# Kernel tuning notes

Measured on AMD Instinct MI355X. Metric: run time of the kernel, lower is better.

## Reference

```python
import jax, jax.numpy as jnp
import numpy as np
from jax import lax


def _conv(x, w):
    # x: [B,H,W,C], w: [kh,kw,Cin,Cout], stride 1, 'same' padding
    return lax.conv_general_dilated(x, w, window_strides=(1, 1), padding='SAME',
                                    dimension_numbers=('NHWC', 'HWIO', 'NHWC'))


def setup_inputs() -> dict:
    key = jax.random.key(0)
    ks = jax.random.split(key, 4)
    B, T, H, W, Cin, F = 16, 5, 256, 256, 3, 8
    return {
        'input_tensor': jax.random.normal(ks[0], (B, T, H, W, Cin), jnp.float32),
        'kernel': jax.random.normal(ks[1], (3, 3, Cin, 4 * F), jnp.float32) * 0.1,
        'recurrent_kernel': jax.random.normal(ks[2], (3, 3, F, 4 * F), jnp.float32) * 0.1,
        'bias': jnp.zeros((4 * F,), jnp.float32),
        'gamma': jnp.ones((F,), jnp.float32),
        'beta': jnp.zeros((F,), jnp.float32),
        'moving_mean': jnp.zeros((F,), jnp.float32),
        'moving_var': jnp.ones((F,), jnp.float32),
        'dense_w': jax.random.normal(ks[3], (F, 2), jnp.float32) * 0.1,
        'dense_b': jnp.zeros((2,), jnp.float32),
    }


def reference(input_tensor, kernel, recurrent_kernel, bias, gamma, beta,
              moving_mean, moving_var, dense_w, dense_b):
    B, T, H, W, Cin = input_tensor.shape
    F = recurrent_kernel.shape[2]
    xs = jnp.moveaxis(input_tensor, 1, 0)  # [T,B,H,W,Cin] time-major for scan
    h0 = jnp.zeros((B, H, W, F), input_tensor.dtype)

    def step(carry, x_t):
        h, c = carry
        # fused 4-gate pre-activations, Keras gate order: i, f, c(g), o
        z = _conv(x_t, kernel) + _conv(h, recurrent_kernel) + bias
        i, f, g, o = jnp.split(z, 4, axis=-1)
        i = jax.nn.sigmoid(i)
        f = jax.nn.sigmoid(f)
        g = jnp.tanh(g)
        o = jax.nn.sigmoid(o)
        c = f * c + i * g
        h = o * jnp.tanh(c)
        return (h, c), None

    (h, _), _ = lax.scan(step, (h0, h0), xs)  # return_sequences=False -> last h

    # BatchNormalization (inference, Keras eps=1e-3)
    eps = 1e-3
    x = (h - moving_mean) * lax.rsqrt(moving_var + eps) * gamma + beta
    # LeakyReLU, Keras default alpha=0.3
    x = jnp.where(x >= 0, x, 0.3 * x)
    # Dense(2) over channel dim
    return jnp.einsum('bhwf,fk->bhwk', x, dense_w) + dense_b
```

## Files before the change

kernel.cpp:

```cpp
#include <hip/hip_runtime.h>


#define BB  16
#define TT  5
#define HH  256
#define WW  256
#define CIN 3
#define FF  8
#define GG  32

#define TW  32
#define THT 16
#define LW  34
#define LH  18
#define NG  8

#define LOG2E 1.44269504088896340736f

typedef _Float16 half8  __attribute__((ext_vector_type(8)));
typedef _Float16 half4  __attribute__((ext_vector_type(4)));
typedef _Float16 half2t __attribute__((ext_vector_type(2)));
typedef float    floatx4 __attribute__((ext_vector_type(4)));

__device__ __forceinline__ float frcp(float x) { return __builtin_amdgcn_rcpf(x); }
__device__ __forceinline__ float sig2(float z)  { return frcp(1.0f + __builtin_amdgcn_exp2f(z)); }
__device__ __forceinline__ float tanh2(float z) { return 1.0f - 2.0f * frcp(1.0f + __builtin_amdgcn_exp2f(z)); }

#define MFMA(A, B, C) __builtin_amdgcn_mfma_f32_16x16x32_f16((A), (B), (C), 0, 0, 0)

__global__ void build_frags(const float* __restrict__ wk,
                            const float* __restrict__ wr,
                            _Float16* __restrict__ blob) {
    const int lane = threadIdx.x & 63;
    const int quad = lane >> 4, nlo = lane & 15;
    for (int chunk = 0; chunk < 5; ++chunk) {
        for (int nh = 0; nh < 2; ++nh) {
            const int n = nh * 16 + nlo;
            const float scale = (n >= 16 && n < 24) ? (2.0f * LOG2E) : (-LOG2E);
            const int frag = chunk * 2 + nh;
            _Float16* dhi = blob + ((size_t)frag * 64 + lane) * 8;
            _Float16* dlo = (chunk >= 2)
                ? blob + ((size_t)(10 + (chunk - 2) * 2 + nh) * 64 + lane) * 8
                : nullptr;
            for (int j = 0; j < 8; ++j) {
                const int k = quad * 8 + j;
                float w = 0.0f;
                if (chunk == 0) {
                    int tap = k >> 2, ci = k & 3;
                    if (ci < 3) w = wk[(tap * 3 + ci) * GG + n];
                } else if (chunk == 1) {
                    if (quad == 0 && j < 3) w = wk[(8 * 3 + j) * GG + n];
                } else {
                    int c = chunk - 2;
                    int tap = c * 4 + quad, ci = j;
                    if (tap < 9) w = wr[(tap * FF + ci) * GG + n];
                }
                w *= scale;
                _Float16 wh = (_Float16)w;
                dhi[j] = wh;
                if (dlo) dlo[j] = (_Float16)(w - (float)wh);
            }
        }
    }
}

template <int MODE>
__global__ __launch_bounds__(256, 2) void lstm_step(
    const float* __restrict__ xg,
    int t,
    const _Float16* __restrict__ blob,
    const float* __restrict__ bias,
    const _Float16* __restrict__ hin,
    _Float16* __restrict__ hout,
    _Float16* __restrict__ cbuf,
    const float* __restrict__ gamma, const float* __restrict__ beta,
    const float* __restrict__ mean,  const float* __restrict__ var,
    const float* __restrict__ dw,    const float* __restrict__ db,
    float* __restrict__ out)
{
    __shared__ half8 hls[LH * LW];
    __shared__ half4 xls[LH * LW];

    const int tid  = threadIdx.x;
    const int bx = blockIdx.x, by = blockIdx.y, b = blockIdx.z;
    const int lane = tid & 63, wave = tid >> 6;
    const int quad = lane >> 4, nlo = lane & 15;
    const bool lo8 = (nlo < 8);
    const int fc = nlo & 7;

    const int gidbase = (((b * (int)gridDim.y + by) * (int)gridDim.x + bx) * 4 + wave) * NG;

    half2t cpre[NG];
    if (MODE != 0) {
#pragma unroll
        for (int g = 0; g < NG; ++g)
            cpre[g] = ((const half2t*)cbuf)[(size_t)(gidbase + g) * 64 + lane];
    }

    half8 bfh[10], bfl[6];
#pragma unroll
    for (int i = 0; i < 10; ++i)
        bfh[i] = *(const half8*)(blob + ((size_t)i * 64 + lane) * 8);
#pragma unroll
    for (int i = 0; i < 6; ++i)
        bfl[i] = *(const half8*)(blob + ((size_t)(10 + i) * 64 + lane) * 8);

    const float bv0 = bias[nlo] * (-LOG2E);
    const float bv1 = bias[16 + nlo] * (lo8 ? 2.0f * LOG2E : -LOG2E);

    for (int l = tid; l < LH * LW; l += 256) {
        int r = l / LW, c = l - r * LW;
        int gy = by * THT + r - 1, gx = bx * TW + c - 1;
        half4 vh = {(_Float16)0, (_Float16)0, (_Float16)0, (_Float16)0};
        if ((unsigned)gy < HH && (unsigned)gx < WW) {
            const float* p = xg + (((size_t)(b * TT + t) * HH + gy) * WW + gx) * CIN;
            vh.x = (_Float16)p[0]; vh.y = (_Float16)p[1]; vh.z = (_Float16)p[2];
        }
        xls[l] = vh;
    }
    if (MODE != 0) {
        for (int l = tid; l < LH * LW; l += 256) {
            int r = l / LW, c = l - r * LW;
            int gy = by * THT + r - 1, gx = bx * TW + c - 1;
            half8 v = {(_Float16)0, (_Float16)0, (_Float16)0, (_Float16)0,
                       (_Float16)0, (_Float16)0, (_Float16)0, (_Float16)0};
            if ((unsigned)gy < HH && (unsigned)gx < WW)
                v = *(const half8*)(hin + ((size_t)(b * HH + gy) * WW + gx) * FF);
            hls[l] = v;
        }
    }
    __syncthreads();

    float bn_s = 0.f, bn_b = 0.f, dw0 = 0.f, dw1 = 0.f, db0 = 0.f, db1 = 0.f;
    if (MODE == 2) {
        bn_s = gamma[fc] * rsqrtf(var[fc] + 1e-3f);
        bn_b = beta[fc] - mean[fc] * bn_s;
        dw0 = dw[fc * 2 + 0]; dw1 = dw[fc * 2 + 1];
        db0 = db[0]; db1 = db[1];
    }

#pragma unroll
    for (int g = 0; g < NG; ++g) {
        const int lr  = wave * 4 + (g >> 1);
        const int gx0 = (g & 1) * 16;
        const int lc  = gx0 + nlo;

        const int t0 = 2 * quad, t1 = t0 + 1;
        half4 p = xls[(lr + t0 / 3) * LW + lc + t0 % 3];
        half4 q = xls[(lr + t1 / 3) * LW + lc + t1 % 3];
        half4 s = xls[(lr + 2) * LW + lc + 2];
        half8 a_xA = (half8){p.x, p.y, p.z, p.w, q.x, q.y, q.z, q.w};
        half8 a_xB = (half8){s.x, s.y, s.z, s.w, s.x, s.y, s.z, s.w};

        floatx4 acc0 = {bv0, bv0, bv0, bv0};
        floatx4 acc1 = {bv1, bv1, bv1, bv1};
        acc0 = MFMA(a_xA, bfh[0], acc0);  acc1 = MFMA(a_xA, bfh[1], acc1);
        acc0 = MFMA(a_xB, bfh[2], acc0);  acc1 = MFMA(a_xB, bfh[3], acc1);
        if (MODE != 0) {
#pragma unroll
            for (int c = 0; c < 3; ++c) {
                int tap = c * 4 + quad;
                if (tap > 8) tap = 8;
                half8 ah = hls[(lr + tap / 3) * LW + lc + tap % 3];
                acc0 = MFMA(ah, bfh[4 + c * 2], acc0);
                acc1 = MFMA(ah, bfh[5 + c * 2], acc1);
                acc0 = MFMA(ah, bfl[c * 2 + 0], acc0);
                acc1 = MFMA(ah, bfl[c * 2 + 1], acc1);
            }
        }

        float s0 = lo8 ? acc0[2] : acc0[0]; float r0 = __shfl_xor(s0, 8, 64);
        float s1 = lo8 ? acc0[3] : acc0[1]; float r1 = __shfl_xor(s1, 8, 64);
        float s2 = lo8 ? acc1[2] : acc1[0]; float r2 = __shfl_xor(s2, 8, 64);
        float s3 = lo8 ? acc1[3] : acc1[1]; float r3 = __shfl_xor(s3, 8, 64);

        const float zi0 = lo8 ? acc0[0] : r0, zi1 = lo8 ? acc0[1] : r1;
        const float zf0 = lo8 ? r0 : acc0[2], zf1 = lo8 ? r1 : acc0[3];
        const float zg0 = lo8 ? acc1[0] : r2, zg1 = lo8 ? acc1[1] : r3;
        const float zo0 = lo8 ? r2 : acc1[2], zo1 = lo8 ? r3 : acc1[3];

        float c0 = 0.f, c1 = 0.f;
        if (MODE != 0) { c0 = (float)cpre[g].x; c1 = (float)cpre[g].y; }

        const float ii0 = sig2(zi0), ff0 = sig2(zf0), gg0 = tanh2(zg0), oo0 = sig2(zo0);
        const float cn0 = ff0 * c0 + ii0 * gg0;
        const float hn0 = oo0 * tanh2(cn0 * (2.0f * LOG2E));
        const float ii1 = sig2(zi1), ff1 = sig2(zf1), gg1 = tanh2(zg1), oo1 = sig2(zo1);
        const float cn1 = ff1 * c1 + ii1 * gg1;
        const float hn1 = oo1 * tanh2(cn1 * (2.0f * LOG2E));

        const int m0 = quad * 4 + (lo8 ? 0 : 2);
        const int gy = by * THT + lr;
        if (MODE != 2) {
            half2t cc; cc.x = (_Float16)cn0; cc.y = (_Float16)cn1;
            ((half2t*)cbuf)[(size_t)(gidbase + g) * 64 + lane] = cc;
            _Float16* hp = hout + ((size_t)(b * HH + gy) * WW + bx * TW + gx0 + m0) * FF + fc;
            hp[0]  = (_Float16)hn0;
            hp[FF] = (_Float16)hn1;
        } else {
            float y0 = bn_s * hn0 + bn_b; y0 = (y0 >= 0.f) ? y0 : 0.3f * y0;
            float y1 = bn_s * hn1 + bn_b; y1 = (y1 >= 0.f) ? y1 : 0.3f * y1;
            float p00 = y0 * dw0, p01 = y0 * dw1;
            float p10 = y1 * dw0, p11 = y1 * dw1;
#pragma unroll
            for (int m = 1; m <= 4; m <<= 1) {
                p00 += __shfl_xor(p00, m, 64);
                p01 += __shfl_xor(p01, m, 64);
                p10 += __shfl_xor(p10, m, 64);
                p11 += __shfl_xor(p11, m, 64);
            }
            const int j = nlo & 7;
            if (j < 4) {
                const int px = m0 + (j >> 1);
                const int k  = j & 1;
                float val = (j == 0 ? p00 : j == 1 ? p01 : j == 2 ? p10 : p11)
                            + (k ? db1 : db0);
                out[((size_t)(b * HH + gy) * WW + bx * TW + gx0 + px) * 2 + k] = val;
            }
        }
    }
}

extern "C" void kernel_launch(void* const* d_in, const int* in_sizes, int n_in,
                              void* d_out, int out_size, void* d_ws, size_t ws_size,
                              hipStream_t stream) {
    const float* x     = (const float*)d_in[0];
    const float* wk    = (const float*)d_in[1];
    const float* wr    = (const float*)d_in[2];
    const float* bias  = (const float*)d_in[3];
    const float* gamma = (const float*)d_in[4];
    const float* beta  = (const float*)d_in[5];
    const float* mean  = (const float*)d_in[6];
    const float* var   = (const float*)d_in[7];
    const float* dw    = (const float*)d_in[8];
    const float* db    = (const float*)d_in[9];
    float* out = (float*)d_out;

    const size_t state = (size_t)BB * HH * WW * FF;
    _Float16* blob = (_Float16*)d_ws;
    _Float16* cbuf = (_Float16*)((char*)d_ws + 32768);
    _Float16* h0   = (_Float16*)((char*)cbuf + state * 2);
    _Float16* h1   = (_Float16*)((char*)h0 + state * 2);

    build_frags<<<1, 64, 0, stream>>>(wk, wr, blob);

    dim3 grid(WW / TW, HH / THT, BB);
    dim3 block(256);
    _Float16* bufs[2] = {h0, h1};
    lstm_step<0><<<grid, block, 0, stream>>>(x, 0, blob, bias, h0, bufs[1], cbuf,
                                             gamma, beta, mean, var, dw, db, out);
    for (int t = 1; t < TT - 1; ++t)
        lstm_step<1><<<grid, block, 0, stream>>>(x, t, blob, bias, bufs[t & 1],
                                                 bufs[(t + 1) & 1], cbuf,
                                                 gamma, beta, mean, var, dw, db, out);
    lstm_step<2><<<grid, block, 0, stream>>>(x, TT - 1, blob, bias, bufs[(TT - 1) & 1],
                                             nullptr, cbuf,
                                             gamma, beta, mean, var, dw, db, out);
}
```

Before: 263.3 us.

## Fuse all LSTM timesteps into one kernel with halo recompute in LDS

Replaces the five per-timestep launches with one kernel that runs all timesteps in a loop. Hidden state lives in double-buffered shared memory, and cell state stays in registers. Each block computes an enlarged region with a 4-pixel halo, so neighbour dependencies are handled by recomputation instead of a grid-wide exchange through global memory. This removes the global h/c reads and writes and the extra launches. The cost is about twice the MFMA and transcendental work from the halo and from the overlapping 16-wide column strips, plus heavier register use.

```diff
diff --git a/kernel.cpp b/kernel.cpp
--- a/kernel.cpp
+++ b/kernel.cpp
@@ -9,17 +9,18 @@
 #define FF  8
 #define GG  32
 
-#define TW  32
-#define THT 16
-#define LW  34
-#define LH  18
-#define NG  8
+#define TWO 32
+#define THO 16
+#define RW  40
+#define RH  24
+#define LWW 42
+#define LHH 26
+#define NR  6
 
 #define LOG2E 1.44269504088896340736f
 
 typedef _Float16 half8  __attribute__((ext_vector_type(8)));
 typedef _Float16 half4  __attribute__((ext_vector_type(4)));
-typedef _Float16 half2t __attribute__((ext_vector_type(2)));
 typedef float    floatx4 __attribute__((ext_vector_type(4)));
 
 __device__ __forceinline__ float frcp(float x) { return __builtin_amdgcn_rcpf(x); }
@@ -64,22 +65,18 @@
     }
 }
 
-template <int MODE>
-__global__ __launch_bounds__(256, 2) void lstm_step(
+__global__ __launch_bounds__(256) void lstm_fused(
     const float* __restrict__ xg,
-    int t,
     const _Float16* __restrict__ blob,
     const float* __restrict__ bias,
-    const _Float16* __restrict__ hin,
-    _Float16* __restrict__ hout,
-    _Float16* __restrict__ cbuf,
     const float* __restrict__ gamma, const float* __restrict__ beta,
     const float* __restrict__ mean,  const float* __restrict__ var,
     const float* __restrict__ dw,    const float* __restrict__ db,
     float* __restrict__ out)
 {
-    __shared__ half8 hls[LH * LW];
-    __shared__ half4 xls[LH * LW];
+    __shared__ half8 hAs[LHH * LWW];
+    __shared__ half8 hBs[LHH * LWW];
+    __shared__ half4 xls[LHH * LWW];
 
     const int tid  = threadIdx.x;
     const int bx = blockIdx.x, by = blockIdx.y, b = blockIdx.z;
@@ -88,15 +85,6 @@
     const bool lo8 = (nlo < 8);
     const int fc = nlo & 7;
 
-    const int gidbase = (((b * (int)gridDim.y + by) * (int)gridDim.x + bx) * 4 + wave) * NG;
-
-    half2t cpre[NG];
-    if (MODE != 0) {
-#pragma unroll
-        for (int g = 0; g < NG; ++g)
-            cpre[g] = ((const half2t*)cbuf)[(size_t)(gidbase + g) * 64 + lane];
-    }
-
     half8 bfh[10], bfl[6];
 #pragma unroll
     for (int i = 0; i < 10; ++i)
@@ -108,116 +96,127 @@
     const float bv0 = bias[nlo] * (-LOG2E);
     const float bv1 = bias[16 + nlo] * (lo8 ? 2.0f * LOG2E : -LOG2E);
 
-    for (int l = tid; l < LH * LW; l += 256) {
-        int r = l / LW, c = l - r * LW;
-        int gy = by * THT + r - 1, gx = bx * TW + c - 1;
-        half4 vh = {(_Float16)0, (_Float16)0, (_Float16)0, (_Float16)0};
-        if ((unsigned)gy < HH && (unsigned)gx < WW) {
-            const float* p = xg + (((size_t)(b * TT + t) * HH + gy) * WW + gx) * CIN;
-            vh.x = (_Float16)p[0]; vh.y = (_Float16)p[1]; vh.z = (_Float16)p[2];
+    const float bn_s = gamma[fc] * rsqrtf(var[fc] + 1e-3f);
+    const float bn_b = beta[fc] - mean[fc] * bn_s;
+    const float dw0 = dw[fc * 2 + 0], dw1 = dw[fc * 2 + 1];
+    const float db0 = db[0], db1 = db[1];
+
+    const half8 hz = {(_Float16)0, (_Float16)0, (_Float16)0, (_Float16)0,
+                      (_Float16)0, (_Float16)0, (_Float16)0, (_Float16)0};
+    for (int l = tid; l < LHH * LWW; l += 256) { hAs[l] = hz; hBs[l] = hz; }
+
+    float c0r[NR][3], c1r[NR][3];
+#pragma unroll
+    for (int r = 0; r < NR; ++r)
+#pragma unroll
+        for (int s = 0; s < 3; ++s) { c0r[r][s] = 0.f; c1r[r][s] = 0.f; }
+
+    for (int t = 0; t < TT; ++t) {
+        half8* hRd = (t & 1) ? hAs : hBs;
+        half8* hWr = (t & 1) ? hBs : hAs;
+
+        for (int l = tid; l < LHH * LWW; l += 256) {
+            int rr = l / LWW, rc = l - rr * LWW;
+            int iy = by * THO + rr - 5;
+            int ix = bx * TWO + rc - 5;
+            half4 vh = {(_Float16)0, (_Float16)0, (_Float16)0, (_Float16)0};
+            if ((unsigned)iy < HH && (unsigned)ix < WW) {
+                const float* p = xg + (((size_t)(b * TT + t) * HH + iy) * WW + ix) * CIN;
+                vh.x = (_Float16)p[0]; vh.y = (_Float16)p[1]; vh.z = (_Float16)p[2];
+            }
+            xls[l] = vh;
         }
-        xls[l] = vh;
-    }
-    if (MODE != 0) {
-        for (int l = tid; l < LH * LW; l += 256) {
-            int r = l / LW, c = l - r * LW;
-            int gy = by * THT + r - 1, gx = bx * TW + c - 1;
-            half8 v = {(_Float16)0, (_Float16)0, (_Float16)0, (_Float16)0,
-                       (_Float16)0, (_Float16)0, (_Float16)0, (_Float16)0};
-            if ((unsigned)gy < HH && (unsigned)gx < WW)
-                v = *(const half8*)(hin + ((size_t)(b * HH + gy) * WW + gx) * FF);
-            hls[l] = v;
-        }
-    }
-    __syncthreads();
-
-    float bn_s = 0.f, bn_b = 0.f, dw0 = 0.f, dw1 = 0.f, db0 = 0.f, db1 = 0.f;
-    if (MODE == 2) {
-        bn_s = gamma[fc] * rsqrtf(var[fc] + 1e-3f);
-        bn_b = beta[fc] - mean[fc] * bn_s;
-        dw0 = dw[fc * 2 + 0]; dw1 = dw[fc * 2 + 1];
-        db0 = db[0]; db1 = db[1];
-    }
-
-#pragma unroll
-    for (int g = 0; g < NG; ++g) {
-        const int lr  = wave * 4 + (g >> 1);
-        const int gx0 = (g & 1) * 16;
-        const int lc  = gx0 + nlo;
-
-        const int t0 = 2 * quad, t1 = t0 + 1;
-        half4 p = xls[(lr + t0 / 3) * LW + lc + t0 % 3];
-        half4 q = xls[(lr + t1 / 3) * LW + lc + t1 % 3];
-        half4 s = xls[(lr + 2) * LW + lc + 2];
-        half8 a_xA = (half8){p.x, p.y, p.z, p.w, q.x, q.y, q.z, q.w};
-        half8 a_xB = (half8){s.x, s.y, s.z, s.w, s.x, s.y, s.z, s.w};
-
-        floatx4 acc0 = {bv0, bv0, bv0, bv0};
-        floatx4 acc1 = {bv1, bv1, bv1, bv1};
-        acc0 = MFMA(a_xA, bfh[0], acc0);  acc1 = MFMA(a_xA, bfh[1], acc1);
-        acc0 = MFMA(a_xB, bfh[2], acc0);  acc1 = MFMA(a_xB, bfh[3], acc1);
-        if (MODE != 0) {
-#pragma unroll
-            for (int c = 0; c < 3; ++c) {
-                int tap = c * 4 + quad;
-                if (tap > 8) tap = 8;
-                half8 ah = hls[(lr + tap / 3) * LW + lc + tap % 3];
-                acc0 = MFMA(ah, bfh[4 + c * 2], acc0);
-                acc1 = MFMA(ah, bfh[5 + c * 2], acc1);
-                acc0 = MFMA(ah, bfl[c * 2 + 0], acc0);
-                acc1 = MFMA(ah, bfl[c * 2 + 1], acc1);
+        __syncthreads();
+
+#pragma unroll
+        for (int r6 = 0; r6 < NR; ++r6) {
+            const int row = wave * NR + r6;
+#pragma unroll
+            for (int s = 0; s < 3; ++s) {
+                const int gx0 = s * 12;
+                const int lc  = gx0 + nlo;
+
+                const int t0 = 2 * quad, t1 = t0 + 1;
+                half4 p = xls[(row + t0 / 3) * LWW + lc + t0 % 3];
+                half4 q = xls[(row + t1 / 3) * LWW + lc + t1 % 3];
+                half4 sx = xls[(row + 2) * LWW + lc + 2];
+                half8 a_xA = (half8){p.x, p.y, p.z, p.w, q.x, q.y, q.z, q.w};
+                half8 a_xB = (half8){sx.x, sx.y, sx.z, sx.w, sx.x, sx.y, sx.z, sx.w};
+
+                floatx4 acc0 = {bv0, bv0, bv0, bv0};
+                floatx4 acc1 = {bv1, bv1, bv1, bv1};
+                acc0 = MFMA(a_xA, bfh[0], acc0);  acc1 = MFMA(a_xA, bfh[1], acc1);
+                acc0 = MFMA(a_xB, bfh[2], acc0);  acc1 = MFMA(a_xB, bfh[3], acc1);
+                if (t > 0) {
+#pragma unroll
+                    for (int c = 0; c < 3; ++c) {
+                        int tap = c * 4 + quad;
+                        if (tap > 8) tap = 8;
+                        half8 ah = hRd[(row + tap / 3) * LWW + lc + tap % 3];
+                        acc0 = MFMA(ah, bfh[4 + c * 2], acc0);
+                        acc1 = MFMA(ah, bfh[5 + c * 2], acc1);
+                        acc0 = MFMA(ah, bfl[c * 2 + 0], acc0);
+                        acc1 = MFMA(ah, bfl[c * 2 + 1], acc1);
+                    }
+                }
+
+                float s0 = lo8 ? acc0[2] : acc0[0]; float r0 = __shfl_xor(s0, 8, 64);
+                float s1 = lo8 ? acc0[3] : acc0[1]; float r1 = __shfl_xor(s1, 8, 64);
+                float s2 = lo8 ? acc1[2] : acc1[0]; float r2 = __shfl_xor(s2, 8, 64);
+                float s3 = lo8 ? acc1[3] : acc1[1]; float r3 = __shfl_xor(s3, 8, 64);
+
+                const float zi0 = lo8 ? acc0[0] : r0, zi1 = lo8 ? acc0[1] : r1;
+                const float zf0 = lo8 ? r0 : acc0[2], zf1 = lo8 ? r1 : acc0[3];
+                const float zg0 = lo8 ? acc1[0] : r2, zg1 = lo8 ? acc1[1] : r3;
+                const float zo0 = lo8 ? r2 : acc1[2], zo1 = lo8 ? r3 : acc1[3];
+
+                const float ii0 = sig2(zi0), ff0 = sig2(zf0), gg0 = tanh2(zg0), oo0 = sig2(zo0);
+                const float cn0 = ff0 * c0r[r6][s] + ii0 * gg0;
+                const float hn0 = oo0 * tanh2(cn0 * (2.0f * LOG2E));
+                const float ii1 = sig2(zi1), ff1 = sig2(zf1), gg1 = tanh2(zg1), oo1 = sig2(zo1);
+                const float cn1 = ff1 * c1r[r6][s] + ii1 * gg1;
+                const float hn1 = oo1 * tanh2(cn1 * (2.0f * LOG2E));
+                c0r[r6][s] = cn0; c1r[r6][s] = cn1;
+
+                const int m0 = quad * 4 + (lo8 ? 0 : 2);
+                const int iy  = by * THO + row - 4;
+                const int ix0 = bx * TWO + gx0 + m0 - 4;
+                if (t < TT - 1) {
+                    const bool iny = (unsigned)iy < HH;
+                    const int idx = (row + 1) * LWW + (gx0 + m0 + 1);
+                    _Float16* hp = (_Float16*)hWr;
+                    hp[idx * 8 + fc] =
+                        (iny && (unsigned)ix0 < WW) ? (_Float16)hn0 : (_Float16)0;
+                    hp[(idx + 1) * 8 + fc] =
+                        (iny && (unsigned)(ix0 + 1) < WW) ? (_Float16)hn1 : (_Float16)0;
+                } else {
+                    float y0 = bn_s * hn0 + bn_b; y0 = (y0 >= 0.f) ? y0 : 0.3f * y0;
+                    float y1 = bn_s * hn1 + bn_b; y1 = (y1 >= 0.f) ? y1 : 0.3f * y1;
+                    float p00 = y0 * dw0, p01 = y0 * dw1;
+                    float p10 = y1 * dw0, p11 = y1 * dw1;
+#pragma unroll
+                    for (int m = 1; m <= 4; m <<= 1) {
+                        p00 += __shfl_xor(p00, m, 64);
+                        p01 += __shfl_xor(p01, m, 64);
+                        p10 += __shfl_xor(p10, m, 64);
+                        p11 += __shfl_xor(p11, m, 64);
+                    }
+                    const int j = nlo & 7;
+                    if (j < 4) {
+                        const int rc = gx0 + m0 + (j >> 1);
+                        const int k  = j & 1;
+                        if (rc >= 4 && rc < 36 && row >= 4 && row < 20) {
+                            const int ox = bx * TWO + rc - 4;
+                            const int oy = by * THO + row - 4;
+                            float val = (j == 0 ? p00 : j == 1 ? p01 : j == 2 ? p10 : p11)
+                                        + (k ? db1 : db0);
+                            out[((size_t)(b * HH + oy) * WW + ox) * 2 + k] = val;
+                        }
+                    }
+                }
             }
         }
-
-        float s0 = lo8 ? acc0[2] : acc0[0]; float r0 = __shfl_xor(s0, 8, 64);
-        float s1 = lo8 ? acc0[3] : acc0[1]; float r1 = __shfl_xor(s1, 8, 64);
-        float s2 = lo8 ? acc1[2] : acc1[0]; float r2 = __shfl_xor(s2, 8, 64);
-        float s3 = lo8 ? acc1[3] : acc1[1]; float r3 = __shfl_xor(s3, 8, 64);
-
-        const float zi0 = lo8 ? acc0[0] : r0, zi1 = lo8 ? acc0[1] : r1;
-        const float zf0 = lo8 ? r0 : acc0[2], zf1 = lo8 ? r1 : acc0[3];
-        const float zg0 = lo8 ? acc1[0] : r2, zg1 = lo8 ? acc1[1] : r3;
-        const float zo0 = lo8 ? r2 : acc1[2], zo1 = lo8 ? r3 : acc1[3];
-
-        float c0 = 0.f, c1 = 0.f;
-        if (MODE != 0) { c0 = (float)cpre[g].x; c1 = (float)cpre[g].y; }
-
-        const float ii0 = sig2(zi0), ff0 = sig2(zf0), gg0 = tanh2(zg0), oo0 = sig2(zo0);
-        const float cn0 = ff0 * c0 + ii0 * gg0;
-        const float hn0 = oo0 * tanh2(cn0 * (2.0f * LOG2E));
-        const float ii1 = sig2(zi1), ff1 = sig2(zf1), gg1 = tanh2(zg1), oo1 = sig2(zo1);
-        const float cn1 = ff1 * c1 + ii1 * gg1;
-        const float hn1 = oo1 * tanh2(cn1 * (2.0f * LOG2E));
-
-        const int m0 = quad * 4 + (lo8 ? 0 : 2);
-        const int gy = by * THT + lr;
-        if (MODE != 2) {
-            half2t cc; cc.x = (_Float16)cn0; cc.y = (_Float16)cn1;
-            ((half2t*)cbuf)[(size_t)(gidbase + g) * 64 + lane] = cc;
-            _Float16* hp = hout + ((size_t)(b * HH + gy) * WW + bx * TW + gx0 + m0) * FF + fc;
-            hp[0]  = (_Float16)hn0;
-            hp[FF] = (_Float16)hn1;
-        } else {
-            float y0 = bn_s * hn0 + bn_b; y0 = (y0 >= 0.f) ? y0 : 0.3f * y0;
-            float y1 = bn_s * hn1 + bn_b; y1 = (y1 >= 0.f) ? y1 : 0.3f * y1;
-            float p00 = y0 * dw0, p01 = y0 * dw1;
-            float p10 = y1 * dw0, p11 = y1 * dw1;
-#pragma unroll
-            for (int m = 1; m <= 4; m <<= 1) {
-                p00 += __shfl_xor(p00, m, 64);
-                p01 += __shfl_xor(p01, m, 64);
-                p10 += __shfl_xor(p10, m, 64);
-                p11 += __shfl_xor(p11, m, 64);
-            }
-            const int j = nlo & 7;
-            if (j < 4) {
-                const int px = m0 + (j >> 1);
-                const int k  = j & 1;
-                float val = (j == 0 ? p00 : j == 1 ? p01 : j == 2 ? p10 : p11)
-                            + (k ? db1 : db0);
-                out[((size_t)(b * HH + gy) * WW + bx * TW + gx0 + px) * 2 + k] = val;
-            }
-        }
+        __syncthreads();
     }
 }
 
@@ -236,24 +235,12 @@
     const float* db    = (const float*)d_in[9];
     float* out = (float*)d_out;
 
-    const size_t state = (size_t)BB * HH * WW * FF;
     _Float16* blob = (_Float16*)d_ws;
-    _Float16* cbuf = (_Float16*)((char*)d_ws + 32768);
-    _Float16* h0   = (_Float16*)((char*)cbuf + state * 2);
-    _Float16* h1   = (_Float16*)((char*)h0 + state * 2);
 
     build_frags<<<1, 64, 0, stream>>>(wk, wr, blob);
 
-    dim3 grid(WW / TW, HH / THT, BB);
+    dim3 grid(WW / TWO, HH / THO, BB);
     dim3 block(256);
-    _Float16* bufs[2] = {h0, h1};
-    lstm_step<0><<<grid, block, 0, stream>>>(x, 0, blob, bias, h0, bufs[1], cbuf,
-                                             gamma, beta, mean, var, dw, db, out);
-    for (int t = 1; t < TT - 1; ++t)
-        lstm_step<1><<<grid, block, 0, stream>>>(x, t, blob, bias, bufs[t & 1],
-                                                 bufs[(t + 1) & 1], cbuf,
-                                                 gamma, beta, mean, var, dw, db, out);
-    lstm_step<2><<<grid, block, 0, stream>>>(x, TT - 1, blob, bias, bufs[(TT - 1) & 1],
-                                             nullptr, cbuf,
-                                             gamma, beta, mean, var, dw, db, out);
+    lstm_fused<<<grid, block, 0, stream>>>(
+        x, blob, bias, gamma, beta, mean, var, dw, db, out);
 }
```

New measurement: 346.1 us. 31.4% more time.
